# Performance work log

Measured on AMD Instinct MI355X. Metric: run time of the kernel, lower is better.

Reference implementation:

```python
import jax, jax.numpy as jnp
import numpy as np

B, N, F, T = 16, 2048, 64, 32  # batch, nodes, features, frames


def setup_inputs() -> dict:
    key = jax.random.key(0)
    ks = jax.random.split(key, 6)
    return {
        "x": jax.random.normal(ks[0], (B, N, F, T), dtype=jnp.float32),
        "U_1": jax.random.normal(ks[1], (N,), dtype=jnp.float32),
        "U_2": jax.random.normal(ks[2], (F, N), dtype=jnp.float32),
        "U_3": jax.random.normal(ks[3], (F,), dtype=jnp.float32),
        "b_e": jax.random.normal(ks[4], (1, T, T), dtype=jnp.float32),
        "V_e": jax.random.normal(ks[5], (T, T), dtype=jnp.float32),
    }


def reference(x, U_1, U_2, U_3, b_e, V_e):
    # lhs = x.permute(0,3,2,1) @ U_1 @ U_2 : (B,T,F,N)@(N,)->(B,T,F); @(F,N)->(B,T,N)
    lhs = jnp.einsum("bnft,n->btf", x, U_1)
    lhs = jnp.einsum("btf,fm->btm", lhs, U_2)
    # rhs = U_3 @ x.permute(2,0,1,3) : (F,)@(F,B,N,T) -> (B,N,T)
    rhs = jnp.einsum("f,bnft->bnt", U_3, x)
    # product : (B,T,N) @ (B,N,T) -> (B,T,T)
    product = jnp.einsum("btn,bns->bts", lhs, rhs)
    # the two chained permutes in the source compose to identity
    E = jnp.einsum("ut,bts->bus", V_e, jax.nn.sigmoid(product + b_e))  # (B,T,T)
    # stable softmax-like normalization over dim=1 (the original's intent)
    E = E - jnp.max(E, axis=1, keepdims=True)
    expE = jnp.exp(E)
    return expE / jnp.sum(expE, axis=1, keepdims=True)
```

## Files before the change

### kernel.cpp

```cpp
#include <hip/hip_runtime.h>
#include <math.h>


#define BDIM 16
#define NDIM 2048
#define FDIM 64
#define TDIM 32
#define GPB  32

__global__ __launch_bounds__(256) void k1_pass(
    const float* __restrict__ x, const float* __restrict__ U1,
    const float* __restrict__ U3, float* __restrict__ rhs_ws,
    float* __restrict__ lhs_part) {
  const int b    = blockIdx.x / GPB;
  const int gb   = blockIdx.x % GPB;
  const int tid  = threadIdx.x;
  const int wave = tid >> 6;
  const int lane = tid & 63;
  const int frow = lane >> 3;
  const int t4   = (lane & 7) * 4;

  float u3v[8];
#pragma unroll
  for (int i = 0; i < 8; ++i) u3v[i] = U3[frow + 8 * i];

  float4 lacc[8];
#pragma unroll
  for (int i = 0; i < 8; ++i) lacc[i] = make_float4(0.f, 0.f, 0.f, 0.f);

  const int wb = gb * 4 + wave;
  for (int n = wb; n < NDIM; n += GPB * 4) {
    const float* base = x + ((size_t)(b * NDIM + n)) * (FDIM * TDIM);
    const float u1n = U1[n];
    float4 racc = make_float4(0.f, 0.f, 0.f, 0.f);
#pragma unroll
    for (int i = 0; i < 8; ++i) {
      const float4 v = *(const float4*)(base + (frow + 8 * i) * TDIM + t4);
      lacc[i].x = fmaf(u1n, v.x, lacc[i].x);
      lacc[i].y = fmaf(u1n, v.y, lacc[i].y);
      lacc[i].z = fmaf(u1n, v.z, lacc[i].z);
      lacc[i].w = fmaf(u1n, v.w, lacc[i].w);
      racc.x = fmaf(u3v[i], v.x, racc.x);
      racc.y = fmaf(u3v[i], v.y, racc.y);
      racc.z = fmaf(u3v[i], v.z, racc.z);
      racc.w = fmaf(u3v[i], v.w, racc.w);
    }
#pragma unroll
    for (int m = 8; m <= 32; m <<= 1) {
      racc.x += __shfl_xor(racc.x, m, 64);
      racc.y += __shfl_xor(racc.y, m, 64);
      racc.z += __shfl_xor(racc.z, m, 64);
      racc.w += __shfl_xor(racc.w, m, 64);
    }
    if (frow == 0) {
      *(float4*)(rhs_ws + ((size_t)(b * NDIM + n)) * TDIM + t4) = racc;
    }
  }

  __shared__ float sred[4 * 2048];
  float* my = sred + wave * 2048;
#pragma unroll
  for (int i = 0; i < 8; ++i)
    *(float4*)(my + (frow + 8 * i) * TDIM + t4) = lacc[i];
  __syncthreads();
  float* outp = lhs_part + ((size_t)(b * GPB + gb)) * 2048;
  for (int p = tid; p < 2048; p += 256)
    outp[p] = sred[p] + sred[2048 + p] + sred[4096 + p] + sred[6144 + p];
}

__global__ __launch_bounds__(256) void k2a(const float* __restrict__ lhs_part,
                                           float* __restrict__ lhs1) {
  const int pos = blockIdx.x * 256 + threadIdx.x;
  const int b = pos >> 11;
  const int p = pos & 2047;
  const float* src = lhs_part + (size_t)b * GPB * 2048 + p;
  float s = 0.f;
#pragma unroll
  for (int g = 0; g < GPB; ++g) s += src[g * 2048];
  lhs1[pos] = s;
}

__global__ __launch_bounds__(256) void k2b(const float* __restrict__ rhs_ws,
                                           const float* __restrict__ U2,
                                           float* __restrict__ R2) {
  const int b  = blockIdx.x >> 3;
  const int fg = blockIdx.x & 7;
  const int tid = threadIdx.x;
  const int c = tid >> 5;
  const int t = tid & 31;
  float acc[8];
#pragma unroll
  for (int i = 0; i < 8; ++i) acc[i] = 0.f;
  const float* rbase = rhs_ws + (size_t)b * NDIM * TDIM;
  for (int i = 0; i < 256; ++i) {
    const int n = c * 256 + i;
    const float v = rbase[n * 32 + t];
#pragma unroll
    for (int fi = 0; fi < 8; ++fi)
      acc[fi] = fmaf(U2[(fg * 8 + fi) * NDIM + n], v, acc[fi]);
  }
  __shared__ float sred[8 * 8 * 32];
#pragma unroll
  for (int fi = 0; fi < 8; ++fi) sred[(c * 8 + fi) * 32 + t] = acc[fi];
  __syncthreads();
  const int fi = tid >> 5, tt = tid & 31;
  float s = 0.f;
#pragma unroll
  for (int cc = 0; cc < 8; ++cc) s += sred[(cc * 8 + fi) * 32 + tt];
  R2[(size_t)b * 2048 + (fg * 8 + fi) * 32 + tt] = s;
}

__global__ __launch_bounds__(1024) void k3(const float* __restrict__ lhs1,
                                           const float* __restrict__ R2,
                                           const float* __restrict__ b_e,
                                           const float* __restrict__ V_e,
                                           float* __restrict__ out) {
  const int b = blockIdx.x;
  const int tid = threadIdx.x;
  __shared__ float sl[2048], sr[2048], sS[1024], sE[1024], sVe[1024], sbe[1024];
  __shared__ float smax[32], ssum[32];
  for (int i = tid; i < 2048; i += 1024) {
    sl[i] = lhs1[b * 2048 + i];
    sr[i] = R2[b * 2048 + i];
  }
  if (tid < 1024) { sVe[tid] = V_e[tid]; sbe[tid] = b_e[tid]; }
  __syncthreads();
  const int t = tid >> 5, s = tid & 31;
  float p = 0.f;
#pragma unroll
  for (int f = 0; f < 64; ++f) p = fmaf(sl[f * 32 + t], sr[f * 32 + s], p);
  sS[t * 32 + s] = 1.f / (1.f + expf(-(p + sbe[t * 32 + s])));
  __syncthreads();
  float e = 0.f;
#pragma unroll
  for (int tt = 0; tt < 32; ++tt) e = fmaf(sVe[t * 32 + tt], sS[tt * 32 + s], e);
  sE[t * 32 + s] = e;
  __syncthreads();
  if (tid < 32) {
    float m = -1e30f;
    for (int uu = 0; uu < 32; ++uu) m = fmaxf(m, sE[uu * 32 + tid]);
    float sum = 0.f;
    for (int uu = 0; uu < 32; ++uu) sum += expf(sE[uu * 32 + tid] - m);
    smax[tid] = m;
    ssum[tid] = sum;
  }
  __syncthreads();
  out[b * 1024 + t * 32 + s] = expf(sE[t * 32 + s] - smax[s]) / ssum[s];
}

extern "C" void kernel_launch(void* const* d_in, const int* in_sizes, int n_in,
                              void* d_out, int out_size, void* d_ws, size_t ws_size,
                              hipStream_t stream) {
  const float* x   = (const float*)d_in[0];
  const float* U1  = (const float*)d_in[1];
  const float* U2  = (const float*)d_in[2];
  const float* U3  = (const float*)d_in[3];
  const float* b_e = (const float*)d_in[4];
  const float* V_e = (const float*)d_in[5];
  float* out = (float*)d_out;
  float* ws  = (float*)d_ws;

  float* rhs_ws   = ws;
  float* lhs_part = ws + 1048576;
  float* lhs1     = ws + 2097152;
  float* R2       = ws + 2097152 + 32768;

  k1_pass<<<BDIM * GPB, 256, 0, stream>>>(x, U1, U3, rhs_ws, lhs_part);
  k2a<<<128, 256, 0, stream>>>(lhs_part, lhs1);
  k2b<<<BDIM * 8, 256, 0, stream>>>(rhs_ws, U2, R2);
  k3<<<BDIM, 1024, 0, stream>>>(lhs1, R2, b_e, V_e, out);
}
```

Baseline: 408.9 us.

## Fuse reduction, U2 projection and epilogue kernels; double k1 grid partitioning

Merges the lhs partial-sum reduction, the rhs-by-U2 projection and the final sigmoid/V_e/softmax stage into a single per-batch kernel with 1024 threads, removing two launches and the intermediate workspace round trips. It also doubles the number of partial groups per batch in the first pass, giving more blocks to stream x with. The cost is that the U2 projection now runs on only 16 blocks, each thread looping serially over all 2048 nodes. The lhs partial buffer also grows, so the final reduction has more partials to sum.

```diff
diff --git a/kernel.cpp b/kernel.cpp
--- a/kernel.cpp
+++ b/kernel.cpp
@@ -6,7 +6,7 @@
 #define NDIM 2048
 #define FDIM 64
 #define TDIM 32
-#define GPB  32
+#define GPB  64
 
 __global__ __launch_bounds__(256) void k1_pass(
     const float* __restrict__ x, const float* __restrict__ U1,
@@ -68,67 +68,46 @@
     outp[p] = sred[p] + sred[2048 + p] + sred[4096 + p] + sred[6144 + p];
 }
 
-__global__ __launch_bounds__(256) void k2a(const float* __restrict__ lhs_part,
-                                           float* __restrict__ lhs1) {
-  const int pos = blockIdx.x * 256 + threadIdx.x;
-  const int b = pos >> 11;
-  const int p = pos & 2047;
-  const float* src = lhs_part + (size_t)b * GPB * 2048 + p;
-  float s = 0.f;
-#pragma unroll
-  for (int g = 0; g < GPB; ++g) s += src[g * 2048];
-  lhs1[pos] = s;
-}
-
-__global__ __launch_bounds__(256) void k2b(const float* __restrict__ rhs_ws,
-                                           const float* __restrict__ U2,
-                                           float* __restrict__ R2) {
-  const int b  = blockIdx.x >> 3;
-  const int fg = blockIdx.x & 7;
-  const int tid = threadIdx.x;
-  const int c = tid >> 5;
-  const int t = tid & 31;
-  float acc[8];
-#pragma unroll
-  for (int i = 0; i < 8; ++i) acc[i] = 0.f;
-  const float* rbase = rhs_ws + (size_t)b * NDIM * TDIM;
-  for (int i = 0; i < 256; ++i) {
-    const int n = c * 256 + i;
-    const float v = rbase[n * 32 + t];
-#pragma unroll
-    for (int fi = 0; fi < 8; ++fi)
-      acc[fi] = fmaf(U2[(fg * 8 + fi) * NDIM + n], v, acc[fi]);
-  }
-  __shared__ float sred[8 * 8 * 32];
-#pragma unroll
-  for (int fi = 0; fi < 8; ++fi) sred[(c * 8 + fi) * 32 + t] = acc[fi];
-  __syncthreads();
-  const int fi = tid >> 5, tt = tid & 31;
-  float s = 0.f;
-#pragma unroll
-  for (int cc = 0; cc < 8; ++cc) s += sred[(cc * 8 + fi) * 32 + tt];
-  R2[(size_t)b * 2048 + (fg * 8 + fi) * 32 + tt] = s;
-}
-
-__global__ __launch_bounds__(1024) void k3(const float* __restrict__ lhs1,
-                                           const float* __restrict__ R2,
-                                           const float* __restrict__ b_e,
-                                           const float* __restrict__ V_e,
-                                           float* __restrict__ out) {
+__global__ __launch_bounds__(1024) void k2_fused(
+    const float* __restrict__ lhs_part, const float* __restrict__ rhs_ws,
+    const float* __restrict__ U2, const float* __restrict__ b_e,
+    const float* __restrict__ V_e, float* __restrict__ out) {
   const int b = blockIdx.x;
   const int tid = threadIdx.x;
-  __shared__ float sl[2048], sr[2048], sS[1024], sE[1024], sVe[1024], sbe[1024];
+  __shared__ float sl[2048];
+  __shared__ float sR[2048];
+  __shared__ float sS[1024], sE[1024], sVe[1024], sbe[1024];
   __shared__ float smax[32], ssum[32];
-  for (int i = tid; i < 2048; i += 1024) {
-    sl[i] = lhs1[b * 2048 + i];
-    sr[i] = R2[b * 2048 + i];
+
+  for (int p = tid; p < 2048; p += 1024) {
+    const float* src = lhs_part + (size_t)b * GPB * 2048 + p;
+    float s = 0.f;
+#pragma unroll
+    for (int g = 0; g < GPB; ++g) s += src[g * 2048];
+    sl[p] = s;
   }
-  if (tid < 1024) { sVe[tid] = V_e[tid]; sbe[tid] = b_e[tid]; }
+  sVe[tid] = V_e[tid];
+  sbe[tid] = b_e[tid];
+
+  const int f2 = tid >> 5, s = tid & 31;
+  const float* rbase = rhs_ws + (size_t)b * NDIM * TDIM;
+  const float* u2a = U2 + (size_t)f2 * NDIM;
+  const float* u2b = U2 + (size_t)(f2 + 32) * NDIM;
+  float a0 = 0.f, a1 = 0.f;
+#pragma unroll 8
+  for (int n = 0; n < NDIM; ++n) {
+    const float v = rbase[n * TDIM + s];
+    a0 = fmaf(u2a[n], v, a0);
+    a1 = fmaf(u2b[n], v, a1);
+  }
+  sR[f2 * 32 + s] = a0;
+  sR[(f2 + 32) * 32 + s] = a1;
   __syncthreads();
-  const int t = tid >> 5, s = tid & 31;
+
+  const int t = tid >> 5;
   float p = 0.f;
 #pragma unroll
-  for (int f = 0; f < 64; ++f) p = fmaf(sl[f * 32 + t], sr[f * 32 + s], p);
+  for (int f = 0; f < FDIM; ++f) p = fmaf(sl[f * 32 + t], sR[f * 32 + s], p);
   sS[t * 32 + s] = 1.f / (1.f + expf(-(p + sbe[t * 32 + s])));
   __syncthreads();
   float e = 0.f;
@@ -162,11 +141,7 @@
 
   float* rhs_ws   = ws;
   float* lhs_part = ws + 1048576;
-  float* lhs1     = ws + 2097152;
-  float* R2       = ws + 2097152 + 32768;
 
   k1_pass<<<BDIM * GPB, 256, 0, stream>>>(x, U1, U3, rhs_ws, lhs_part);
-  k2a<<<128, 256, 0, stream>>>(lhs_part, lhs1);
-  k2b<<<BDIM * 8, 256, 0, stream>>>(rhs_ws, U2, R2);
-  k3<<<BDIM, 1024, 0, stream>>>(lhs1, R2, b_e, V_e, out);
+  k2_fused<<<BDIM, 1024, 0, stream>>>(lhs_part, rhs_ws, U2, b_e, V_e, out);
 }
```

New measurement: 558.8 us. +36.7%, slower.
